# Kernel tuning notes

Measured on AMD Instinct MI355X. Metric: run time of the kernel, lower is better.

The kernel has to match this reference:

```python
import jax, jax.numpy as jnp
from jax import lax
import numpy as np

# ----- static optical constants (from config) -----
N = 500            # phase mask grid
PX = 1e-6          # pixel pitch [m]
WL = 532e-9        # wavelength [m]
FL = 0.1           # focal length [m]
RI = 1.0           # refractive index
FWHC = 150e-6      # laser beam FWHC
K = 2.0 * np.pi * RI / WL
QE, DARK_MEAN, READ_STD, GAIN, MAX_ADU = 0.9, 0.005, 1.6, 2.0, 65535.0
MAX_VAL = 4.0e9    # Normalize01 max
PHOTONS = 1.0e6    # photons per emitter (max_intensity-style scaling)
R = 15             # psf_keep_radius -> 31x31 crops

_x = np.arange(-N // 2, N // 2) * PX
_X, _Y = np.meshgrid(_x, _x)
INCIDENT = np.exp(-(_X**2 + _Y**2) / (2.0 * FWHC**2)).astype(np.float32)
_C1 = (np.pi / (WL * FL) * (_X**2 + _Y**2)) % (2.0 * np.pi)
B1 = np.exp(-1j * _C1).astype(np.complex64)
# angular-spectrum gamma, directly in unshifted fft order
_F = np.fft.fftfreq(N, d=PX)
_A, _B = np.meshgrid(RI * WL * _F, RI * WL * _F)
GAMMA = np.sqrt(np.maximum(1.0 - _A**2 - _B**2, 0.0)).astype(np.float32)

def _gauss7():
    m = (7 - 1) / 2.0
    y, x = np.ogrid[-m:m + 1, -m:m + 1]
    h = np.exp(-(x * x + y * y) / 2.0)
    h[h < np.finfo(h.dtype).eps * h.max()] = 0
    return h.astype(np.float32)
GAUSS7 = _gauss7()


def setup_inputs() -> dict:
    key = jax.random.key(0)
    k1, k2, k3, k4, k5, k6, k7 = jax.random.split(key, 7)
    B, Ne = 8, 64
    phase_mask = jax.random.uniform(k1, (N, N), jnp.float32, 0.0, 2.0 * np.pi)
    zs = jax.random.uniform(k2, (Ne,), jnp.float32, 0.0, 1e-4)  # defocus depths [m]
    xyz = jax.random.randint(k3, (B, Ne, 2), 0, 170, jnp.int32) + 15  # in [15,184]
    std_u = jax.random.uniform(k4, (1,), jnp.float32)
    eps_dark = jax.random.normal(k5, (B, 1, 198, 198), jnp.float32)
    eps_photon = jax.random.normal(k6, (B, 1, 198, 198), jnp.float32)
    eps_read = jax.random.normal(k7, (B, 1, 198, 198), jnp.float32)
    return {"phase_mask": phase_mask, "zs": zs, "xyz": xyz, "std_u": std_u,
            "eps_dark": eps_dark, "eps_photon": eps_photon, "eps_read": eps_read}


def _forward(phase_mask, zs, xyz, std_u, eps_dark, eps_photon, eps_read):
    Bn, Ne = xyz.shape[0], xyz.shape[1]
    # --- FFT-based PSF generation (angular spectrum propagation) ---
    field = (INCIDENT * jnp.exp(1j * phase_mask) * B1).astype(jnp.complex64)  # [N,N]
    Ef = jnp.fft.fft2(field)                                                  # [N,N]
    H = jnp.exp(1j * ((K * GAMMA)[None] * zs[:, None, None]))                 # [Ne,N,N]
    Eprop = jnp.fft.ifft2(Ef[None] * H)                                       # [Ne,N,N]
    inten = jnp.abs(Eprop) ** 2
    c = N // 2
    psf = inten[:, c - R:c + R + 1, c - R:c + R + 1]                          # [Ne,31,31]
    psf = psf / (jnp.sum(psf, (-2, -1), keepdims=True) + 1e-12) * PHOTONS
    images4D = jnp.broadcast_to(psf[None], (Bn, Ne, 2 * R + 1, 2 * R + 1))
    # --- imgs4dto3d: scatter-add 31x31 patches into 200x200 canvas ---
    offs = jnp.arange(2 * R + 1) - R
    rows = xyz[..., 0][..., None, None] + offs[None, None, :, None]           # [B,Ne,31,1]
    cols = xyz[..., 1][..., None, None] + offs[None, None, None, :]           # [B,Ne,1,31]
    bidx = jnp.arange(Bn)[:, None, None, None]
    canvas = jnp.zeros((Bn, 200, 200), psf.dtype).at[bidx, rows, cols].add(images4D)
    img = canvas[:, None]                                                     # [B,1,200,200]
    # --- BlurLayer: per-draw std gaussian, conv pad=2 -> 198x198 ---
    std = 0.8 + 0.4 * std_u[0]
    s2 = std * std
    kern = (1.0 / (2.0 * jnp.pi * s2)) * GAUSS7 ** (1.0 / s2)
    blurred = lax.conv_general_dilated(img, kern[None, None], (1, 1),
                                       [(2, 2), (2, 2)],
                                       dimension_numbers=("NCHW", "OIHW", "NCHW"))
    # --- NoiseLayer (reparameterized gaussian approximations) ---
    sig = blurred * QE
    dark = DARK_MEAN + eps_dark * jnp.sqrt(jnp.float32(DARK_MEAN))
    total = jnp.maximum(sig + dark, 0.0)
    noisy = total + eps_photon * jnp.sqrt(jnp.maximum(total, 1e-12))
    elec = noisy + eps_read * READ_STD
    adu = jnp.clip(elec * GAIN, 0.0, MAX_ADU)
    # --- Normalize01 ---
    out = jnp.where(adu <= 10.0, 1.0, jnp.minimum(adu, MAX_VAL)) / MAX_VAL
    return out.astype(jnp.float32)


def reference(phase_mask, zs, xyz, std_u, eps_dark, eps_photon, eps_read):
    return _forward(phase_mask, zs, xyz, std_u, eps_dark, eps_photon, eps_read)
```

## Files before the change

kernel.cpp:

```cpp
#include <hip/hip_runtime.h>
#include <math.h>

#define NN 500
#define NE 64
#define BATCH 8
#define RR 15
#define PW 31
#define CAN 200
#define OHW 198
#define TWO_PI_F 6.28318530717958647692f
#define SETUP_N (BATCH * CAN * CAN + NE + 49)

#define BCH 8
#define BKC 128
#define BSTR 136
#define BG_CHUNK (2 * 64 * BSTR)
#define ASCALE (1.0f / 64.0f)

using f16x8 = __attribute__((ext_vector_type(8))) _Float16;
using f32x4 = __attribute__((ext_vector_type(4))) float;

__device__ __forceinline__ void fast_sincos_red(float theta, float* s, float* c) {
    const float INV2PI = 0.15915494309189535f;
    const float PI2_HI = 6.28318548202514648f;
    const float PI2_LO = -1.7484556e-7f;
    float n = rintf(theta * INV2PI);
    float r = fmaf(n, -PI2_HI, theta);
    r = fmaf(n, -PI2_LO, r);
    *s = __sinf(r);
    *c = __cosf(r);
}

__global__ void k_setup(const float* __restrict__ std_u,
                        float* __restrict__ kgamma,
                        float2* __restrict__ tw,
                        float* __restrict__ kern,
                        float* __restrict__ canvas,
                        float* __restrict__ psf_sums) {
    int idx = blockIdx.x * blockDim.x + threadIdx.x;
    if (idx < NN) {
        double th = 2.0 * M_PI * (double)idx / (double)NN;
        tw[idx] = make_float2((float)cos(th), (float)sin(th));
    }
    if (idx < BATCH * CAN * CAN) canvas[idx] = 0.f;
    if (idx >= BATCH * CAN * CAN && idx < BATCH * CAN * CAN + NE)
        psf_sums[idx - BATCH * CAN * CAN] = 0.f;
    if (idx >= BATCH * CAN * CAN + NE && idx < SETUP_N) {
        int t = idx - (BATCH * CAN * CAN + NE);
        float stdv = 0.8f + 0.4f * std_u[0];
        float s2 = stdv * stdv;
        int a = t / 7 - 3, b = t % 7 - 3;
        float g = (float)exp(-0.5 * (double)(a * a + b * b));
        kern[t] = (1.0f / (2.0f * (float)M_PI * s2)) * powf(g, 1.0f / s2);
    }
    if (idx >= NN * NN) return;
    int i = idx / NN, j = idx % NN;
    double fy = (double)((i < 250) ? i : i - 500) * 2000.0;
    double fx = (double)((j < 250) ? j : j - 500) * 2000.0;
    double a = 5.32e-7 * fx;
    double b = 5.32e-7 * fy;
    double g = 1.0 - a * a - b * b;
    g = (g > 0.0) ? sqrt(g) : 0.0;
    float Kf = (float)(2.0 * M_PI * 1.0 / 5.32e-7);
    kgamma[idx] = Kf * (float)g;
}

__global__ void k_setup_b(_Float16* __restrict__ Bg) {
    int idx = blockIdx.x * blockDim.x + threadIdx.x;
    if (idx >= BCH * 64 * BSTR) return;
    int c = idx / (64 * BSTR);
    int rem = idx % (64 * BSTR);
    int nu = rem / BSTR, j = rem % BSTR;
    float hi = 0.f, lo = 0.f;
    int kap = c * BKC + j;
    if (j < BKC && kap < 2 * NN) {
        int u = kap >> 1, p = kap & 1;
        int ri = nu >> 1, q = nu & 1;
        int r = 235 + ri;
        int m = (u * r) % NN;
        double th = 2.0 * M_PI * (double)m / (double)NN;
        double wre = cos(th), wim = sin(th);
        double val = (q == 0) ? ((p == 0) ? wre : -wim)
                              : ((p == 0) ? wim : wre);
        float x = (float)val;
        _Float16 h = (_Float16)x;
        hi = (float)h;
        lo = x - (float)h;
    }
    size_t base = (size_t)c * BG_CHUNK + (size_t)nu * BSTR + j;
    Bg[base] = (_Float16)hi;
    Bg[base + (size_t)64 * BSTR] = (_Float16)lo;
}

__device__ __forceinline__ void ct_dft_stages(const float2* xs, const float2* tts,
                                              float2* S, int t,
                                              float2* out1, float2* out2, int* kout) {
    if (t < 250) {
        int d = t / 25;
        int b = t % 25;
        float2 st = tts[(25 * d) % NN];
        float wr = 1.f, wi = 0.f;
        float Er = 0.f, Ei = 0.f, Or_ = 0.f, Oi = 0.f;
#pragma unroll
        for (int a = 0; a < 20; a += 2) {
            float2 x0 = xs[25 * a + b];
            Er += x0.x * wr - x0.y * wi;
            Ei += x0.x * wi + x0.y * wr;
            float nr = wr * st.x - wi * st.y;
            float ni = wr * st.y + wi * st.x;
            float2 x1 = xs[25 * (a + 1) + b];
            Or_ += x1.x * nr - x1.y * ni;
            Oi  += x1.x * ni + x1.y * nr;
            wr = nr * st.x - ni * st.y;
            wi = nr * st.y + ni * st.x;
        }
        S[b * 21 + d]      = make_float2(Er + Or_, Ei + Oi);
        S[b * 21 + d + 10] = make_float2(Er - Or_, Ei - Oi);
    }
    __syncthreads();
    if (t < 250) {
        int k = t;
        int d1 = k % 20;
        int d2 = (d1 + 10) % 20;
        float2 s1 = tts[k];
        float wr = 1.f, wi = 0.f;
        float a1r = 0.f, a1i = 0.f, a2r = 0.f, a2i = 0.f;
#pragma unroll
        for (int b = 0; b < 25; ++b) {
            float2 u1 = S[b * 21 + d1];
            float2 u2 = S[b * 21 + d2];
            a1r += u1.x * wr - u1.y * wi;
            a1i += u1.x * wi + u1.y * wr;
            float sgnb = (b & 1) ? -1.f : 1.f;
            float w2r = sgnb * wr, w2i = sgnb * wi;
            a2r += u2.x * w2r - u2.y * w2i;
            a2i += u2.x * w2i + u2.y * w2r;
            float nr = wr * s1.x - wi * s1.y;
            wi = wr * s1.y + wi * s1.x;
            wr = nr;
        }
        *out1 = make_float2(a1r, a1i);
        *out2 = make_float2(a2r, a2i);
        *kout = k;
    }
}

__global__ void k_dft_rows(const float* __restrict__ phase, float2* __restrict__ dst,
                           const float2* __restrict__ tw) {
    __shared__ __align__(16) float2 xs[NN];
    __shared__ float2 tts[NN];
    __shared__ float2 S[25 * 21];
    int line = blockIdx.x;
    int t = threadIdx.x;
    const float INV2SIG = 2.2222222e7f;
    const float C1M = (float)(M_PI / 5.32e-8);
    float y = (float)(line - 250) * 1e-6f;
    float y2 = y * y;
    const float* prow = phase + (size_t)line * NN;
    for (int n = t; n < NN; n += 256) {
        float x = (float)(n - 250) * 1e-6f;
        float r2 = x * x + y2;
        float inc = __expf(-r2 * INV2SIG);
        float c1 = C1M * r2;
        float b1r = __cosf(c1), b1i = -__sinf(c1);
        float ph = prow[n];
        float sp = __sinf(ph), cp = __cosf(ph);
        float ar = inc * cp, ai = inc * sp;
        xs[n] = make_float2(ar * b1r - ai * b1i, ar * b1i + ai * b1r);
        float2 tt = tw[n];
        tts[n] = make_float2(tt.x, -tt.y);
    }
    __syncthreads();
    float2 o1, o2; int k;
    ct_dft_stages(xs, tts, S, t, &o1, &o2, &k);
    if (t < 250) {
        dst[(size_t)k * NN + line] = o1;
        dst[(size_t)(k + 250) * NN + line] = o2;
    }
}

__global__ void k_dft_cols(const float2* __restrict__ src, float2* __restrict__ dst,
                           const float2* __restrict__ tw) {
    __shared__ __align__(16) float2 xs[NN];
    __shared__ float2 tts[NN];
    __shared__ float2 S[25 * 21];
    int line = blockIdx.x;
    const float2* s = src + (size_t)line * NN;
    int t = threadIdx.x;
    for (int n = t; n < NN; n += 256) {
        xs[n] = s[n];
        float2 tt = tw[n];
        tts[n] = make_float2(tt.x, -tt.y);
    }
    __syncthreads();
    float2 o1, o2; int k;
    ct_dft_stages(xs, tts, S, t, &o1, &o2, &k);
    if (t < 250) {
        float2* dp = dst + (size_t)line * NN;
        dp[k] = o1;
        dp[k + 250] = o2;
    }
}

__global__ void __launch_bounds__(256, 4)
k_prop_mfma(const float2* __restrict__ EfT,
            const float* __restrict__ kgamma,
            const float* __restrict__ zs,
            const _Float16* __restrict__ Bg,
            float2* __restrict__ part) {
    __shared__ __align__(16) _Float16 Bbuf[2][64 * BSTR];
    __shared__ __align__(16) float2 eft[512];
    __shared__ __align__(16) float kgs[512];
    int v = blockIdx.x;
    int t = threadIdx.x;
    int w = t >> 6;
    int lane = t & 63;
    int lrow = lane & 15;
    int grp = lane >> 4;

    for (int n = t; n < 512; n += 256) {
        if (n < NN) {
            eft[n] = EfT[(size_t)v * NN + n];
            kgs[n] = kgamma[(size_t)v * NN + n];
        } else {
            eft[n] = make_float2(0.f, 0.f);
            kgs[n] = 0.f;
        }
    }
    float zv = zs[w * 16 + lrow];

    f32x4 acc[4] = {};

#define MODSPLIT(ex, ey, kgv, i0) do {                                        \
        float s_, c_;                                                         \
        fast_sincos_red((kgv) * zv, &s_, &c_);                                \
        float yr = ((ex) * c_ - (ey) * s_) * ASCALE;                          \
        float yi = ((ex) * s_ + (ey) * c_) * ASCALE;                          \
        _Float16 h0 = (_Float16)yr;                                           \
        ah[i0] = h0; al[i0] = (_Float16)(yr - (float)h0);                     \
        _Float16 h1 = (_Float16)yi;                                           \
        ah[i0 + 1] = h1; al[i0 + 1] = (_Float16)(yi - (float)h1);             \
    } while (0)

    for (int c = 0; c < BCH; ++c) {
        __syncthreads();
        const float4* src = (const float4*)(Bg + (size_t)c * BG_CHUNK);
        float4* dst = (float4*)(&Bbuf[0][0]);
        for (int q2 = t; q2 < BG_CHUNK / 8; q2 += 256)
            dst[q2] = src[q2];
        __syncthreads();

#pragma unroll
        for (int sl = 0; sl < 4; ++sl) {
            int s = c * 4 + sl;
            int u0 = s * 16 + grp * 4;
            float4 e01 = *(const float4*)&eft[u0];
            float4 e23 = *(const float4*)&eft[u0 + 2];
            float4 kg4 = *(const float4*)&kgs[u0];
            f16x8 ah, al;
            MODSPLIT(e01.x, e01.y, kg4.x, 0);
            MODSPLIT(e01.z, e01.w, kg4.y, 2);
            MODSPLIT(e23.x, e23.y, kg4.z, 4);
            MODSPLIT(e23.z, e23.w, kg4.w, 6);
            int koff = sl * 32 + grp * 8;
#pragma unroll
            for (int nt = 0; nt < 4; ++nt) {
                int nu = nt * 16 + lrow;
                f16x8 bh = *(const f16x8*)&Bbuf[0][nu * BSTR + koff];
                f16x8 bl = *(const f16x8*)&Bbuf[1][nu * BSTR + koff];
                acc[nt] = __builtin_amdgcn_mfma_f32_16x16x32_f16(ah, bh, acc[nt], 0, 0, 0);
                acc[nt] = __builtin_amdgcn_mfma_f32_16x16x32_f16(al, bh, acc[nt], 0, 0, 0);
                acc[nt] = __builtin_amdgcn_mfma_f32_16x16x32_f16(ah, bl, acc[nt], 0, 0, 0);
            }
        }
    }
#undef MODSPLIT

    float* pf = (float*)part;
#pragma unroll
    for (int nt = 0; nt < 4; ++nt) {
        int nu = nt * 16 + lrow;
        int ri = nu >> 1, q = nu & 1;
        if (ri < PW) {
#pragma unroll
            for (int rg = 0; rg < 4; ++rg) {
                int z = w * 16 + grp * 4 + rg;
                pf[(((size_t)z * PW + ri) * NN + v) * 2 + q] = acc[nt][rg];
            }
        }
    }
}

__global__ void k_prop_cols(const float2* __restrict__ part,
                            float* __restrict__ psf,
                            float* __restrict__ psf_sums) {
    __shared__ float2 X[NN];
    __shared__ float sred[PW];
    int r = blockIdx.x;
    int z = blockIdx.y;
    int t = threadIdx.x;
    const float2* col = part + ((size_t)z * PW + r) * NN;
    for (int v = t; v < NN; v += 256) X[v] = col[v];
    __syncthreads();
    if (t < PW * 8) {
        int ci = t >> 3, seg = t & 7;
        int c = 235 + ci;
        float wr, wi, sr, si;
        {
            float th0 = (TWO_PI_F / NN) * (float)((seg * c) % NN);
            sincosf(th0, &wi, &wr);
            float ths = (TWO_PI_F / NN) * (float)((8 * c) % NN);
            sincosf(ths, &si, &sr);
        }
        float ar = 0.f, ai = 0.f;
        for (int v = seg; v < NN; v += 8) {
            float2 xv = X[v];
            ar += xv.x * wr - xv.y * wi;
            ai += xv.x * wi + xv.y * wr;
            float nwr = wr * sr - wi * si;
            wi = wr * si + wi * sr;
            wr = nwr;
        }
#pragma unroll
        for (int m = 1; m < 8; m <<= 1) {
            ar += __shfl_xor(ar, m);
            ai += __shfl_xor(ai, m);
        }
        if (seg == 0 && ci < PW) {
            const float inv = 64.0f / 250000.0f;
            float re = ar * inv, im = ai * inv;
            float val = re * re + im * im;
            psf[(size_t)z * (PW * PW) + r * PW + ci] = val;
            sred[ci] = val;
        }
    }
    __syncthreads();
    if (t == 0) {
        float s = 0.f;
#pragma unroll
        for (int i = 0; i < PW; ++i) s += sred[i];
        atomicAdd(&psf_sums[z], s);
    }
}

__global__ void k_scatter(const float* __restrict__ psf,
                          const float* __restrict__ psf_sums,
                          const int* __restrict__ xyz,
                          float* __restrict__ canvas) {
    int e = blockIdx.x;
    int b = blockIdx.y;
    int r0 = xyz[(b * NE + e) * 2 + 0] - RR;
    int c0 = xyz[(b * NE + e) * 2 + 1] - RR;
    float sc = 1.0e6f / (psf_sums[e] + 1e-12f);
    float* cb = canvas + (size_t)b * (CAN * CAN);
    for (int p = threadIdx.x; p < PW * PW; p += blockDim.x) {
        int i = p / PW, j = p % PW;
        atomicAdd(cb + (r0 + i) * CAN + (c0 + j), psf[e * PW * PW + p] * sc);
    }
}

__global__ void k_final(const float* __restrict__ canvas,
                        const float* __restrict__ kern,
                        const float* __restrict__ eps_dark,
                        const float* __restrict__ eps_photon,
                        const float* __restrict__ eps_read,
                        float* __restrict__ out) {
    __shared__ float kk[49];
    __shared__ float tile[14][40];
    int b = blockIdx.z;
    int tx = threadIdx.x, ty = threadIdx.y;
    int t = ty * 32 + tx;
    int j0 = blockIdx.x * 32, i0 = blockIdx.y * 8;
    if (t < 49) kk[t] = kern[t];
    const float* cb = canvas + (size_t)b * (CAN * CAN);
    for (int p = t; p < 14 * 38; p += 256) {
        int rr = p / 38, cc = p % 38;
        int gi = i0 + rr - 2, gj = j0 + cc - 2;
        tile[rr][cc] = (gi >= 0 && gi < CAN && gj >= 0 && gj < CAN)
                           ? cb[gi * CAN + gj] : 0.f;
    }
    __syncthreads();
    int i = i0 + ty, j = j0 + tx;
    if (i >= OHW || j >= OHW) return;
    float acc = 0.f;
#pragma unroll
    for (int a = 0; a < 7; ++a)
#pragma unroll
        for (int q = 0; q < 7; ++q)
            acc += tile[ty + a][tx + q] * kk[a * 7 + q];
    int idx = b * (OHW * OHW) + i * OHW + j;
    float sig = acc * 0.9f;
    float dark = 0.005f + eps_dark[idx] * sqrtf(0.005f);
    float total = fmaxf(sig + dark, 0.0f);
    float noisy = total + eps_photon[idx] * sqrtf(fmaxf(total, 1e-12f));
    float elec = noisy + eps_read[idx] * 1.6f;
    float adu = fminf(fmaxf(elec * 2.0f, 0.0f), 65535.0f);
    float v = (adu <= 10.0f) ? 1.0f : fminf(adu, 4.0e9f);
    out[idx] = v / 4.0e9f;
}

extern "C" void kernel_launch(void* const* d_in, const int* in_sizes, int n_in,
                              void* d_out, int out_size, void* d_ws, size_t ws_size,
                              hipStream_t stream) {
    const float* phase    = (const float*)d_in[0];
    const float* zs       = (const float*)d_in[1];
    const int*   xyz      = (const int*)d_in[2];
    const float* std_u    = (const float*)d_in[3];
    const float* epsd     = (const float*)d_in[4];
    const float* epsp     = (const float*)d_in[5];
    const float* epsr     = (const float*)d_in[6];
    float* out = (float*)d_out;

    char* ws = (char*)d_ws;
    size_t off = 0;
    auto alloc = [&](size_t bytes) {
        off = (off + 255) & ~(size_t)255;
        size_t o = off; off += bytes; return o;
    };
    float*  kgamma   = (float*) (ws + alloc((size_t)NN * NN * 4));
    float2* tw       = (float2*)(ws + alloc((size_t)NN * 8));
    float2* R1T      = (float2*)(ws + alloc((size_t)NN * NN * 8));
    float2* EfT      = (float2*)(ws + alloc((size_t)NN * NN * 8));
    float2* part     = (float2*)(ws + alloc((size_t)NE * PW * NN * 8));
    float*  psf      = (float*) (ws + alloc((size_t)NE * PW * PW * 4));
    float*  psf_sums = (float*) (ws + alloc((size_t)NE * 4));
    float*  kern     = (float*) (ws + alloc((size_t)64 * 4));
    float*  canvas   = (float*) (ws + alloc((size_t)BATCH * CAN * CAN * 4));
    _Float16* Bg     = (_Float16*)(ws + alloc((size_t)BCH * BG_CHUNK * 2));
    (void)ws_size; (void)n_in; (void)in_sizes; (void)out_size;

    k_setup<<<(SETUP_N + 255) / 256, 256, 0, stream>>>(
        std_u, kgamma, tw, kern, canvas, psf_sums);
    k_setup_b<<<(BCH * 64 * BSTR + 255) / 256, 256, 0, stream>>>(Bg);
    k_dft_rows<<<NN, 256, 0, stream>>>(phase, R1T, tw);
    k_dft_cols<<<NN, 256, 0, stream>>>(R1T, EfT, tw);
    k_prop_mfma<<<NN, 256, 0, stream>>>(EfT, kgamma, zs, Bg, part);
    k_prop_cols<<<dim3(PW, NE), 256, 0, stream>>>(part, psf, psf_sums);
    k_scatter<<<dim3(NE, BATCH), 256, 0, stream>>>(psf, psf_sums, xyz, canvas);
    k_final<<<dim3((OHW + 31) / 32, (OHW + 7) / 8, BATCH), dim3(32, 8), 0, stream>>>(
        canvas, kern, epsd, epsp, epsr, out);
}
```

Measured before the change: 160.4 us.

## Process two columns per block and double-buffer B chunks via register staging

```diff
diff --git a/kernel.cpp b/kernel.cpp
--- a/kernel.cpp
+++ b/kernel.cpp
@@ -11,10 +11,11 @@
 #define TWO_PI_F 6.28318530717958647692f
 #define SETUP_N (BATCH * CAN * CAN + NE + 49)
 
-#define BCH 8
-#define BKC 128
-#define BSTR 136
+#define BCH 16
+#define BKC 64
+#define BSTR 72
 #define BG_CHUNK (2 * 64 * BSTR)
+#define NLD (BG_CHUNK * 2 / 16)
 #define ASCALE (1.0f / 64.0f)
 
 using f16x8 = __attribute__((ext_vector_type(8))) _Float16;
@@ -202,77 +203,111 @@
     }
 }
 
-__global__ void __launch_bounds__(256, 4)
+__global__ void __launch_bounds__(256)
 k_prop_mfma(const float2* __restrict__ EfT,
             const float* __restrict__ kgamma,
             const float* __restrict__ zs,
             const _Float16* __restrict__ Bg,
             float2* __restrict__ part) {
-    __shared__ __align__(16) _Float16 Bbuf[2][64 * BSTR];
-    __shared__ __align__(16) float2 eft[512];
-    __shared__ __align__(16) float kgs[512];
-    int v = blockIdx.x;
+    __shared__ __align__(16) _Float16 Bbuf[2][BG_CHUNK];
+    __shared__ __align__(16) float2 eft[2][512];
+    __shared__ __align__(16) float kgs[2][512];
+    int v0 = blockIdx.x * 2;
     int t = threadIdx.x;
     int w = t >> 6;
     int lane = t & 63;
     int lrow = lane & 15;
     int grp = lane >> 4;
 
-    for (int n = t; n < 512; n += 256) {
-        if (n < NN) {
-            eft[n] = EfT[(size_t)v * NN + n];
-            kgs[n] = kgamma[(size_t)v * NN + n];
+    for (int n = t; n < 1024; n += 256) {
+        int vv = n >> 9, u = n & 511;
+        if (u < NN) {
+            eft[vv][u] = EfT[(size_t)(v0 + vv) * NN + u];
+            kgs[vv][u] = kgamma[(size_t)(v0 + vv) * NN + u];
         } else {
-            eft[n] = make_float2(0.f, 0.f);
-            kgs[n] = 0.f;
-        }
+            eft[vv][u] = make_float2(0.f, 0.f);
+            kgs[vv][u] = 0.f;
+        }
+    }
+    {
+        const float4* srcb = (const float4*)Bg;
+        float4* dstb = (float4*)&Bbuf[0][0];
+        for (int i = t; i < NLD; i += 256) dstb[i] = srcb[i];
     }
     float zv = zs[w * 16 + lrow];
-
-    f32x4 acc[4] = {};
-
-#define MODSPLIT(ex, ey, kgv, i0) do {                                        \
+    __syncthreads();
+
+    f32x4 acc0[4] = {};
+    f32x4 acc1[4] = {};
+
+#define MODSPLIT(AH, AL, ex, ey, kgv, i0) do {                                \
         float s_, c_;                                                         \
         fast_sincos_red((kgv) * zv, &s_, &c_);                                \
         float yr = ((ex) * c_ - (ey) * s_) * ASCALE;                          \
         float yi = ((ex) * s_ + (ey) * c_) * ASCALE;                          \
         _Float16 h0 = (_Float16)yr;                                           \
-        ah[i0] = h0; al[i0] = (_Float16)(yr - (float)h0);                     \
+        AH[i0] = h0; AL[i0] = (_Float16)(yr - (float)h0);                     \
         _Float16 h1 = (_Float16)yi;                                           \
-        ah[i0 + 1] = h1; al[i0 + 1] = (_Float16)(yi - (float)h1);             \
+        AH[i0 + 1] = h1; AL[i0 + 1] = (_Float16)(yi - (float)h1);             \
     } while (0)
 
     for (int c = 0; c < BCH; ++c) {
-        __syncthreads();
-        const float4* src = (const float4*)(Bg + (size_t)c * BG_CHUNK);
-        float4* dst = (float4*)(&Bbuf[0][0]);
-        for (int q2 = t; q2 < BG_CHUNK / 8; q2 += 256)
-            dst[q2] = src[q2];
-        __syncthreads();
-
-#pragma unroll
-        for (int sl = 0; sl < 4; ++sl) {
-            int s = c * 4 + sl;
+        float4 stg[5];
+        if (c + 1 < BCH) {
+            const float4* srcb = (const float4*)(Bg + (size_t)(c + 1) * BG_CHUNK);
+#pragma unroll
+            for (int k = 0; k < 5; ++k) {
+                int i = t + k * 256;
+                if (i < NLD) stg[k] = srcb[i];
+            }
+        }
+        const _Float16* Bb = &Bbuf[c & 1][0];
+#pragma unroll
+        for (int sl = 0; sl < 2; ++sl) {
+            int s = c * 2 + sl;
             int u0 = s * 16 + grp * 4;
-            float4 e01 = *(const float4*)&eft[u0];
-            float4 e23 = *(const float4*)&eft[u0 + 2];
-            float4 kg4 = *(const float4*)&kgs[u0];
-            f16x8 ah, al;
-            MODSPLIT(e01.x, e01.y, kg4.x, 0);
-            MODSPLIT(e01.z, e01.w, kg4.y, 2);
-            MODSPLIT(e23.x, e23.y, kg4.z, 4);
-            MODSPLIT(e23.z, e23.w, kg4.w, 6);
+            f16x8 ah0, al0, ah1, al1;
+            {
+                float4 e01 = *(const float4*)&eft[0][u0];
+                float4 e23 = *(const float4*)&eft[0][u0 + 2];
+                float4 kg4 = *(const float4*)&kgs[0][u0];
+                MODSPLIT(ah0, al0, e01.x, e01.y, kg4.x, 0);
+                MODSPLIT(ah0, al0, e01.z, e01.w, kg4.y, 2);
+                MODSPLIT(ah0, al0, e23.x, e23.y, kg4.z, 4);
+                MODSPLIT(ah0, al0, e23.z, e23.w, kg4.w, 6);
+            }
+            {
+                float4 e01 = *(const float4*)&eft[1][u0];
+                float4 e23 = *(const float4*)&eft[1][u0 + 2];
+                float4 kg4 = *(const float4*)&kgs[1][u0];
+                MODSPLIT(ah1, al1, e01.x, e01.y, kg4.x, 0);
+                MODSPLIT(ah1, al1, e01.z, e01.w, kg4.y, 2);
+                MODSPLIT(ah1, al1, e23.x, e23.y, kg4.z, 4);
+                MODSPLIT(ah1, al1, e23.z, e23.w, kg4.w, 6);
+            }
             int koff = sl * 32 + grp * 8;
 #pragma unroll
             for (int nt = 0; nt < 4; ++nt) {
                 int nu = nt * 16 + lrow;
-                f16x8 bh = *(const f16x8*)&Bbuf[0][nu * BSTR + koff];
-                f16x8 bl = *(const f16x8*)&Bbuf[1][nu * BSTR + koff];
-                acc[nt] = __builtin_amdgcn_mfma_f32_16x16x32_f16(ah, bh, acc[nt], 0, 0, 0);
-                acc[nt] = __builtin_amdgcn_mfma_f32_16x16x32_f16(al, bh, acc[nt], 0, 0, 0);
-                acc[nt] = __builtin_amdgcn_mfma_f32_16x16x32_f16(ah, bl, acc[nt], 0, 0, 0);
-            }
-        }
+                f16x8 bh = *(const f16x8*)&Bb[nu * BSTR + koff];
+                f16x8 bl = *(const f16x8*)&Bb[64 * BSTR + nu * BSTR + koff];
+                acc0[nt] = __builtin_amdgcn_mfma_f32_16x16x32_f16(ah0, bh, acc0[nt], 0, 0, 0);
+                acc0[nt] = __builtin_amdgcn_mfma_f32_16x16x32_f16(al0, bh, acc0[nt], 0, 0, 0);
+                acc0[nt] = __builtin_amdgcn_mfma_f32_16x16x32_f16(ah0, bl, acc0[nt], 0, 0, 0);
+                acc1[nt] = __builtin_amdgcn_mfma_f32_16x16x32_f16(ah1, bh, acc1[nt], 0, 0, 0);
+                acc1[nt] = __builtin_amdgcn_mfma_f32_16x16x32_f16(al1, bh, acc1[nt], 0, 0, 0);
+                acc1[nt] = __builtin_amdgcn_mfma_f32_16x16x32_f16(ah1, bl, acc1[nt], 0, 0, 0);
+            }
+        }
+        if (c + 1 < BCH) {
+            float4* dstb = (float4*)&Bbuf[(c + 1) & 1][0];
+#pragma unroll
+            for (int k = 0; k < 5; ++k) {
+                int i = t + k * 256;
+                if (i < NLD) dstb[i] = stg[k];
+            }
+        }
+        __syncthreads();
     }
 #undef MODSPLIT
 
@@ -285,7 +320,9 @@
 #pragma unroll
             for (int rg = 0; rg < 4; ++rg) {
                 int z = w * 16 + grp * 4 + rg;
-                pf[(((size_t)z * PW + ri) * NN + v) * 2 + q] = acc[nt][rg];
+                size_t base = (((size_t)z * PW + ri) * NN) * 2;
+                pf[base + (size_t)v0 * 2 + q]       = acc0[nt][rg];
+                pf[base + (size_t)(v0 + 1) * 2 + q] = acc1[nt][rg];
             }
         }
     }
@@ -434,7 +471,7 @@
     k_setup_b<<<(BCH * 64 * BSTR + 255) / 256, 256, 0, stream>>>(Bg);
     k_dft_rows<<<NN, 256, 0, stream>>>(phase, R1T, tw);
     k_dft_cols<<<NN, 256, 0, stream>>>(R1T, EfT, tw);
-    k_prop_mfma<<<NN, 256, 0, stream>>>(EfT, kgamma, zs, Bg, part);
+    k_prop_mfma<<<NN / 2, 256, 0, stream>>>(EfT, kgamma, zs, Bg, part);
     k_prop_cols<<<dim3(PW, NE), 256, 0, stream>>>(part, psf, psf_sums);
     k_scatter<<<dim3(NE, BATCH), 256, 0, stream>>>(psf, psf_sums, xyz, canvas);
     k_final<<<dim3((OHW + 31) / 32, (OHW + 7) / 8, BATCH), dim3(32, 8), 0, stream>>>(
```

Result: slower. 175.1 us (+9.2%).

## Split MFMA propagation K-range across two blocks and double-buffer B chunks

Applied to the files above, without the earlier changes.

```diff
diff --git a/kernel.cpp b/kernel.cpp
--- a/kernel.cpp
+++ b/kernel.cpp
@@ -11,11 +11,13 @@
 #define TWO_PI_F 6.28318530717958647692f
 #define SETUP_N (BATCH * CAN * CAN + NE + 49)
 
-#define BCH 8
-#define BKC 128
-#define BSTR 136
+#define BCH 16
+#define BKC 64
+#define BSTR 72
 #define BG_CHUNK (2 * 64 * BSTR)
+#define NLD (BG_CHUNK * 2 / 16)
 #define ASCALE (1.0f / 64.0f)
+#define PART_HALF ((size_t)NE * PW * NN)
 
 using f16x8 = __attribute__((ext_vector_type(8))) _Float16;
 using f32x4 = __attribute__((ext_vector_type(4))) float;
@@ -208,26 +210,34 @@
             const float* __restrict__ zs,
             const _Float16* __restrict__ Bg,
             float2* __restrict__ part) {
-    __shared__ __align__(16) _Float16 Bbuf[2][64 * BSTR];
-    __shared__ __align__(16) float2 eft[512];
-    __shared__ __align__(16) float kgs[512];
+    __shared__ __align__(16) _Float16 Bbuf[2][BG_CHUNK];
+    __shared__ __align__(16) float2 eft[256];
+    __shared__ __align__(16) float kgs[256];
     int v = blockIdx.x;
+    int kh = blockIdx.y;
     int t = threadIdx.x;
     int w = t >> 6;
     int lane = t & 63;
     int lrow = lane & 15;
     int grp = lane >> 4;
 
-    for (int n = t; n < 512; n += 256) {
-        if (n < NN) {
-            eft[n] = EfT[(size_t)v * NN + n];
-            kgs[n] = kgamma[(size_t)v * NN + n];
+    {
+        int u = 256 * kh + t;
+        if (u < NN) {
+            eft[t] = EfT[(size_t)v * NN + u];
+            kgs[t] = kgamma[(size_t)v * NN + u];
         } else {
-            eft[n] = make_float2(0.f, 0.f);
-            kgs[n] = 0.f;
-        }
+            eft[t] = make_float2(0.f, 0.f);
+            kgs[t] = 0.f;
+        }
+    }
+    {
+        const float4* srcb = (const float4*)(Bg + (size_t)(8 * kh) * BG_CHUNK);
+        float4* dstb = (float4*)&Bbuf[0][0];
+        for (int i = t; i < NLD; i += 256) dstb[i] = srcb[i];
     }
     float zv = zs[w * 16 + lrow];
+    __syncthreads();
 
     f32x4 acc[4] = {};
 
@@ -242,41 +252,56 @@
         ah[i0 + 1] = h1; al[i0 + 1] = (_Float16)(yi - (float)h1);             \
     } while (0)
 
-    for (int c = 0; c < BCH; ++c) {
-        __syncthreads();
-        const float4* src = (const float4*)(Bg + (size_t)c * BG_CHUNK);
-        float4* dst = (float4*)(&Bbuf[0][0]);
-        for (int q2 = t; q2 < BG_CHUNK / 8; q2 += 256)
-            dst[q2] = src[q2];
-        __syncthreads();
-
-#pragma unroll
-        for (int sl = 0; sl < 4; ++sl) {
-            int s = c * 4 + sl;
-            int u0 = s * 16 + grp * 4;
-            float4 e01 = *(const float4*)&eft[u0];
-            float4 e23 = *(const float4*)&eft[u0 + 2];
-            float4 kg4 = *(const float4*)&kgs[u0];
+    for (int ci = 0; ci < 8; ++ci) {
+        float4 stg[5];
+        if (ci + 1 < 8) {
+            const float4* srcb =
+                (const float4*)(Bg + (size_t)(8 * kh + ci + 1) * BG_CHUNK);
+#pragma unroll
+            for (int k = 0; k < 5; ++k) {
+                int i = t + k * 256;
+                if (i < NLD) stg[k] = srcb[i];
+            }
+        }
+        const _Float16* Bb = &Bbuf[ci & 1][0];
+#pragma unroll
+        for (int sl = 0; sl < 2; ++sl) {
+            int s_loc = ci * 2 + sl;
+            int u0 = s_loc * 16 + grp * 4;
             f16x8 ah, al;
-            MODSPLIT(e01.x, e01.y, kg4.x, 0);
-            MODSPLIT(e01.z, e01.w, kg4.y, 2);
-            MODSPLIT(e23.x, e23.y, kg4.z, 4);
-            MODSPLIT(e23.z, e23.w, kg4.w, 6);
+            {
+                float4 e01 = *(const float4*)&eft[u0];
+                float4 e23 = *(const float4*)&eft[u0 + 2];
+                float4 kg4 = *(const float4*)&kgs[u0];
+                MODSPLIT(e01.x, e01.y, kg4.x, 0);
+                MODSPLIT(e01.z, e01.w, kg4.y, 2);
+                MODSPLIT(e23.x, e23.y, kg4.z, 4);
+                MODSPLIT(e23.z, e23.w, kg4.w, 6);
+            }
             int koff = sl * 32 + grp * 8;
 #pragma unroll
             for (int nt = 0; nt < 4; ++nt) {
                 int nu = nt * 16 + lrow;
-                f16x8 bh = *(const f16x8*)&Bbuf[0][nu * BSTR + koff];
-                f16x8 bl = *(const f16x8*)&Bbuf[1][nu * BSTR + koff];
+                f16x8 bh = *(const f16x8*)&Bb[nu * BSTR + koff];
+                f16x8 bl = *(const f16x8*)&Bb[64 * BSTR + nu * BSTR + koff];
                 acc[nt] = __builtin_amdgcn_mfma_f32_16x16x32_f16(ah, bh, acc[nt], 0, 0, 0);
                 acc[nt] = __builtin_amdgcn_mfma_f32_16x16x32_f16(al, bh, acc[nt], 0, 0, 0);
                 acc[nt] = __builtin_amdgcn_mfma_f32_16x16x32_f16(ah, bl, acc[nt], 0, 0, 0);
             }
         }
+        if (ci + 1 < 8) {
+            float4* dstb = (float4*)&Bbuf[(ci + 1) & 1][0];
+#pragma unroll
+            for (int k = 0; k < 5; ++k) {
+                int i = t + k * 256;
+                if (i < NLD) dstb[i] = stg[k];
+            }
+        }
+        __syncthreads();
     }
 #undef MODSPLIT
 
-    float* pf = (float*)part;
+    float* pf = (float*)(part + (size_t)kh * PART_HALF);
 #pragma unroll
     for (int nt = 0; nt < 4; ++nt) {
         int nu = nt * 16 + lrow;
@@ -299,8 +324,12 @@
     int r = blockIdx.x;
     int z = blockIdx.y;
     int t = threadIdx.x;
-    const float2* col = part + ((size_t)z * PW + r) * NN;
-    for (int v = t; v < NN; v += 256) X[v] = col[v];
+    const float2* col0 = part + ((size_t)z * PW + r) * NN;
+    const float2* col1 = col0 + PART_HALF;
+    for (int v = t; v < NN; v += 256) {
+        float2 a = col0[v], b = col1[v];
+        X[v] = make_float2(a.x + b.x, a.y + b.y);
+    }
     __syncthreads();
     if (t < PW * 8) {
         int ci = t >> 3, seg = t & 7;
@@ -421,7 +450,7 @@
     float2* tw       = (float2*)(ws + alloc((size_t)NN * 8));
     float2* R1T      = (float2*)(ws + alloc((size_t)NN * NN * 8));
     float2* EfT      = (float2*)(ws + alloc((size_t)NN * NN * 8));
-    float2* part     = (float2*)(ws + alloc((size_t)NE * PW * NN * 8));
+    float2* part     = (float2*)(ws + alloc(2 * PART_HALF * 8));
     float*  psf      = (float*) (ws + alloc((size_t)NE * PW * PW * 4));
     float*  psf_sums = (float*) (ws + alloc((size_t)NE * 4));
     float*  kern     = (float*) (ws + alloc((size_t)64 * 4));
@@ -434,7 +463,7 @@
     k_setup_b<<<(BCH * 64 * BSTR + 255) / 256, 256, 0, stream>>>(Bg);
     k_dft_rows<<<NN, 256, 0, stream>>>(phase, R1T, tw);
     k_dft_cols<<<NN, 256, 0, stream>>>(R1T, EfT, tw);
-    k_prop_mfma<<<NN, 256, 0, stream>>>(EfT, kgamma, zs, Bg, part);
+    k_prop_mfma<<<dim3(NN, 2), 256, 0, stream>>>(EfT, kgamma, zs, Bg, part);
     k_prop_cols<<<dim3(PW, NE), 256, 0, stream>>>(part, psf, psf_sums);
     k_scatter<<<dim3(NE, BATCH), 256, 0, stream>>>(psf, psf_sums, xyz, canvas);
     k_final<<<dim3((OHW + 31) / 32, (OHW + 7) / 8, BATCH), dim3(32, 8), 0, stream>>>(
```

Result: slower. 179.3 us (+11.8%).
